# Kernel tuning notes

Hardware: AMD Instinct MI355X
Metric: run time of the kernel (lower is better)

## Reference

```python
import jax, jax.numpy as jnp
import numpy as np

H, KV, D, WIN = 16, 4, 128, 1024


def _rope(x, cos, sin):
    # x: [B, H, S, D]; cos/sin: [1, 1, S, D//2]
    d = x.shape[-1] // 2
    x1, x2 = x[..., :d], x[..., d:]
    S = x.shape[2]
    c, s = cos[:, :, :S], sin[:, :, :S]
    return jnp.concatenate([x1 * c + x2 * s, -x1 * s + x2 * c], axis=-1)


def _rms_norm(x):
    eps = jnp.finfo(x.dtype).eps
    return x * jax.lax.rsqrt(jnp.mean(jnp.square(x), axis=-1, keepdims=True) + eps)


def setup_inputs() -> dict:
    key = jax.random.key(0)
    ks = jax.random.split(key, 7)
    B, S, E = 2, 2048, 2048
    return {
        "x": jax.random.normal(ks[0], (B, S, E), jnp.float32),
        "cos": jax.random.normal(ks[1], (1, 1, S, D // 2), jnp.float32),
        "sin": jax.random.normal(ks[2], (1, 1, S, D // 2), jnp.float32),
        "Wq": jax.random.normal(ks[3], (H * D, E), jnp.float32) * 0.02,
        "Wk": jax.random.normal(ks[4], (KV * D, E), jnp.float32) * 0.02,
        "Wv": jax.random.normal(ks[5], (KV * D, E), jnp.float32) * 0.02,
        "Wo": jax.random.normal(ks[6], (E, H * D), jnp.float32) * 0.02,
    }


def reference(x, cos, sin, Wq, Wk, Wv, Wo):
    B, S, E = x.shape
    rep = H // KV
    # projections -> [B, heads, S, D]
    q = (x @ Wq.T).reshape(B, S, H, D).transpose(0, 2, 1, 3)
    k = (x @ Wk.T).reshape(B, S, KV, D).transpose(0, 2, 1, 3)
    v = (x @ Wv.T).reshape(B, S, KV, D).transpose(0, 2, 1, 3)
    # GQA: materialize repeated K/V heads (matches repeat_interleave)
    k = jnp.repeat(k, rep, axis=1)
    v = jnp.repeat(v, rep, axis=1)
    # RoPE then QK RMSNorm (no learned scale)
    q = _rms_norm(_rope(q, cos, sin))
    k = _rms_norm(_rope(k, cos, sin))
    scores = jnp.einsum("bhqd,bhkd->bhqk", q, k) * (D ** -0.5)
    # causal & sliding-window mask
    i = jnp.arange(S)[:, None]
    j = jnp.arange(S)[None, :]
    mask = (i >= j) & (jnp.abs(i - j) < WIN)
    scores = jnp.where(mask[None, None], scores, -jnp.inf)
    attn = jax.nn.softmax(scores, axis=-1)
    out = jnp.einsum("bhqk,bhkd->bhqd", attn, v)
    out = out.transpose(0, 2, 1, 3).reshape(B, S, H * D)
    return out @ Wo.T
```

## Files before the change

### kernel.cpp

```cpp
#include <hip/hip_runtime.h>
#include <stdint.h>

using bf16 = __bf16;
typedef __bf16 bf16x8 __attribute__((ext_vector_type(8)));
typedef __bf16 bf16x4 __attribute__((ext_vector_type(4)));
typedef float f32x4 __attribute__((ext_vector_type(4)));

#define H_ 16
#define KV_ 4
#define D_ 128
#define WIN_ 1024
#define B_ 2
#define S_ 2048
#define E_ 2048
#define HD_ 2048

__device__ __forceinline__ void gld_lds16(const void* gptr, void* lptr) {
    __builtin_amdgcn_global_load_lds(
        (__attribute__((address_space(1))) void*)(uintptr_t)gptr,
        (__attribute__((address_space(3))) void*)(uintptr_t)lptr, 16, 0, 0);
}

__global__ __launch_bounds__(256) void cvt_all(const float* __restrict__ x,
                                               const float* __restrict__ wq,
                                               const float* __restrict__ wk,
                                               const float* __restrict__ wv,
                                               const float* __restrict__ wo,
                                               bf16* __restrict__ dst) {
    int i = (blockIdx.x * 256 + threadIdx.x) * 4;
    const float* src;
    int off;
    if (i < 8388608)       { src = x;  off = 0; }
    else if (i < 12582912) { src = wq; off = 8388608; }
    else if (i < 13631488) { src = wk; off = 12582912; }
    else if (i < 14680064) { src = wv; off = 13631488; }
    else                   { src = wo; off = 14680064; }
    const float4 v = *(const float4*)(src + (i - off));
    bf16x4 o = {(bf16)v.x, (bf16)v.y, (bf16)v.z, (bf16)v.w};
    *(bf16x4*)(dst + i) = o;
}

#define SCHED0() __builtin_amdgcn_sched_barrier(0)
#define BAR()                          \
    do {                               \
        SCHED0();                      \
        __builtin_amdgcn_s_barrier();  \
        SCHED0();                      \
    } while (0)
#define WAITV(N) asm volatile("s_waitcnt vmcnt(" #N ")" ::: "memory")


template <int NH>
__device__ __forceinline__ void gemm_core32(const bf16* __restrict__ A,
                                            const bf16* __restrict__ W, int m0,
                                            int n0, bf16* sm, f32x4 (&acc)[8][2 * NH]) {
    constexpr int K = 2048;
    const int t = threadIdx.x;
    const int lane = t & 63;
    const int wave = t >> 6;
    const int l15 = lane & 15;
    const int quad = lane >> 4;
    const int wm = (wave & 1) * 128;
    const int wn = (wave >> 1) * (NH * 32);

    bf16* const A0 = sm;
    bf16* const A1 = sm + 8192;
    bf16* const A2 = sm + 16384;
    bf16* const A3 = sm + 24576;
    bf16* const B0 = sm + 32768;
    bf16* const B1 = B0 + NH * 4096;
    bf16* const B2 = B0 + NH * 8192;
    bf16* const B3 = B0 + NH * 12288;

    const bf16* Ap = A + (size_t)(m0 + (t >> 2)) * K + (t & 3) * 8;
    const bf16* Wp = W + (size_t)(n0 + (t >> 2)) * K + (t & 3) * 8;

    auto stA = [&](int u, bf16* d) {
        gld_lds16(Ap + u * 32, d + t * 8);
        gld_lds16(Ap + u * 32 + (size_t)128 * K, d + 4096 + t * 8);
    };
    auto stB = [&](int u, bf16* d) {
        gld_lds16(Wp + u * 32, d + t * 8);
        if constexpr (NH == 2) gld_lds16(Wp + u * 32 + (size_t)128 * K, d + 4096 + t * 8);
    };

    bf16x8 afX[8], afY[8], bfX[2 * NH], bfY[2 * NH];
    auto rdA = [&](const bf16* S, bf16x8 (&af)[8]) {
#pragma unroll
        for (int mi = 0; mi < 8; ++mi)
            af[mi] = *(const bf16x8*)&S[(wm + mi * 16 + l15) * 32 + quad * 8];
    };
    auto rdB = [&](const bf16* S, bf16x8 (&bf)[2 * NH]) {
#pragma unroll
        for (int j = 0; j < 2 * NH; ++j)
            bf[j] = *(const bf16x8*)&S[(wn + j * 16 + l15) * 32 + quad * 8];
    };
    auto MMA = [&](bf16x8 (&af)[8], bf16x8 (&bf)[2 * NH]) {
        __builtin_amdgcn_s_setprio(1);
#pragma unroll
        for (int mi = 0; mi < 8; ++mi)
#pragma unroll
            for (int j = 0; j < 2 * NH; ++j)
                acc[mi][j] = __builtin_amdgcn_mfma_f32_16x16x32_bf16(af[mi], bf[j],
                                                                     acc[mi][j], 0, 0, 0);
        __builtin_amdgcn_s_setprio(0);
    };

#define GT(U, AFM, BFM, AFR, BFR, RA, RB, SA, SB, DOST, WMODE)                      \
    do {                                                                            \
        if (DOST) { stA((U) + 3, SA); stB((U) + 3, SB); }                           \
        MMA(AFM, BFM);                                                              \
        rdA(RA, AFR);                                                               \
        rdB(RB, BFR);                                                               \
        SCHED0();                                                                   \
        if ((WMODE) == 1) {                                                         \
            if constexpr (NH == 2) { WAITV(4); } else { WAITV(3); }                 \
        } else if ((WMODE) == 0) {                                                  \
            WAITV(0);                                                               \
        }                                                                           \
        BAR();                                                                      \
    } while (0)

    stA(0, A0); stB(0, B0);
    stA(1, A1); stB(1, B1);
    stA(2, A2); stB(2, B2);
    SCHED0();
    if constexpr (NH == 2) { WAITV(4); } else { WAITV(3); }
    BAR();
    rdA(A0, afX);
    rdB(B0, bfX);

    for (int it = 0; it < 15; ++it) {
        const int u = it * 4;
        GT(u + 0, afX, bfX, afY, bfY, A1, B1, A3, B3, 1, 1);
        GT(u + 1, afY, bfY, afX, bfX, A2, B2, A0, B0, 1, 1);
        GT(u + 2, afX, bfX, afY, bfY, A3, B3, A1, B1, 1, 1);
        GT(u + 3, afY, bfY, afX, bfX, A0, B0, A2, B2, 1, 1);
    }
    GT(60, afX, bfX, afY, bfY, A1, B1, A3, B3, 1, 1);
    GT(61, afY, bfY, afX, bfX, A2, B2, A0, B0, 0, 0);
    GT(62, afX, bfX, afY, bfY, A3, B3, A1, B1, 0, -1);
    MMA(afY, bfY);
#undef GT
}

__global__ __launch_bounds__(512, 2) void gemm_qkv8(const bf16* __restrict__ A,
                                                    const bf16* __restrict__ W,
                                                    const float* __restrict__ cosp,
                                                    const float* __restrict__ sinp,
                                                    bf16* __restrict__ qn,
                                                    bf16* __restrict__ kn,
                                                    bf16* __restrict__ vt) {
    __shared__ alignas(16) bf16 sm[65536];
    const int flat = blockIdx.y * 16 + blockIdx.x;
    const int swz = (flat & 7) * 24 + (flat >> 3);
    const int m0 = (swz & 15) * 256;
    const int n0 = (swz >> 4) * 256;

    f32x4 acc[8][4] = {};
    gemm_core32<2>(A, W, m0, n0, sm, acc);

    const int t = threadIdx.x;
    const int lane = t & 63;
    const int wave = t >> 6;
    const int l15 = lane & 15;
    const int quad = lane >> 4;
    const int wm = (wave & 1) * 128;
    const int wn = (wave >> 1) * 64;
    bf16* Cs = sm;

#pragma unroll
    for (int ch = 0; ch < 2; ++ch) {
        __syncthreads();
        if (wm == ch * 128) {
#pragma unroll
            for (int mi = 0; mi < 8; ++mi) {
                const int rl = mi * 16 + quad * 4;
#pragma unroll
                for (int nf = 0; nf < 4; ++nf) {
                    const int col = wn + nf * 16 + l15;
#pragma unroll
                    for (int r = 0; r < 4; ++r)
                        Cs[(rl + r) * 264 + col] = (bf16)acc[mi][nf][r];
                }
            }
        }
        __syncthreads();

        if (n0 < 2560) {
            const int rt = t >> 1;
            const int row = rt & 127;
            const int hh = rt >> 7;
            const int half = t & 1;
            const int gr = m0 + ch * 128 + row;
            const int bb = gr >> 11;
            const int s = gr & 2047;
            const int unit = (n0 >> 7) + hh;
            const bf16* crow = &Cs[row * 264 + hh * 128 + half * 32];
            const float* cp = cosp + s * 64 + half * 32;
            const float* sp = sinp + s * 64 + half * 32;
            bf16x8 xa[4], xb2[4];
#pragma unroll
            for (int u = 0; u < 4; ++u) {
                xa[u] = *(const bf16x8*)(crow + u * 8);
                xb2[u] = *(const bf16x8*)(crow + 64 + u * 8);
            }
            float y1[32], y2[32], ss = 0.0f;
#pragma unroll
            for (int u = 0; u < 4; ++u)
#pragma unroll
                for (int e = 0; e < 8; ++e) {
                    const int jj = u * 8 + e;
                    const float x1 = (float)xa[u][e];
                    const float x2 = (float)xb2[u][e];
                    const float c = cp[jj];
                    const float sn = sp[jj];
                    y1[jj] = x1 * c + x2 * sn;
                    y2[jj] = x2 * c - x1 * sn;
                    ss += y1[jj] * y1[jj] + y2[jj] * y2[jj];
                }
            ss += __shfl_xor(ss, 1, 64);
            float rr = rsqrtf(ss * (1.0f / 128.0f) + 1.1920929e-7f);
            bf16* dst;
            if (unit < 16) {
                rr *= 0.12751740f;
                dst = qn + ((size_t)(bb * H_ + unit) * S_ + s) * 128 + half * 32;
            } else {
                dst = kn + ((size_t)(bb * KV_ + (unit - 16)) * S_ + s) * 128 + half * 32;
            }
#pragma unroll
            for (int u = 0; u < 4; ++u) {
                bf16x8 p1, p2;
#pragma unroll
                for (int e = 0; e < 8; ++e) {
                    p1[e] = (bf16)(y1[u * 8 + e] * rr);
                    p2[e] = (bf16)(y2[u * 8 + e] * rr);
                }
                *(bf16x8*)(dst + u * 8) = p1;
                *(bf16x8*)(dst + 64 + u * 8) = p2;
            }
        } else {
            const int hh = t >> 8;
            const int d = (t >> 1) & 127;
            const int sl0 = (t & 1) * 64;
            const int jv = (n0 >> 7) + hh - 20;
            const int base = m0 + ch * 128;
            const int bb = base >> 11;
            const int sW = (base & 2047) + sl0;
            bf16* vdst = vt + ((size_t)(bb * KV_ + jv) * 128 + d) * S_ + sW;
#pragma unroll
            for (int u = 0; u < 8; ++u) {
                bf16x8 pk;
#pragma unroll
                for (int e = 0; e < 8; ++e)
                    pk[e] = Cs[(sl0 + u * 8 + e) * 264 + hh * 128 + d];
                *(bf16x8*)(vdst + u * 8) = pk;
            }
        }
    }
}

__global__ __launch_bounds__(512, 2) void gemm_bt8(const bf16* __restrict__ A,
                                                   const bf16* __restrict__ W,
                                                   float* __restrict__ C, int K,
                                                   int ldc) {
    __shared__ alignas(16) bf16 sm[49152];
    const int flat = blockIdx.y * 16 + blockIdx.x;
    const int swz = (flat & 7) * 32 + (flat >> 3);
    const int m0 = (swz & 15) * 256;
    const int n0 = (swz >> 4) * 128;

    f32x4 acc[8][2] = {};
    gemm_core32<1>(A, W, m0, n0, sm, acc);

    const int t = threadIdx.x;
    const int lane = t & 63;
    const int l15 = lane & 15;
    const int quad = lane >> 4;
    const int wave = t >> 6;
    const int wm = (wave & 1) * 128;
    const int wn = (wave >> 1) * 32;
#pragma unroll
    for (int mi = 0; mi < 8; ++mi) {
        const int row = m0 + wm + mi * 16 + quad * 4;
#pragma unroll
        for (int j = 0; j < 2; ++j) {
            const int col = n0 + wn + j * 16 + l15;
#pragma unroll
            for (int r = 0; r < 4; ++r) C[(size_t)(row + r) * ldc + col] = acc[mi][j][r];
        }
    }
}

__global__ __launch_bounds__(256, 4) void attn_fwd(const bf16* __restrict__ Qn,
                                                   const bf16* __restrict__ Kn,
                                                   const bf16* __restrict__ Vt,
                                                   bf16* __restrict__ Out) {
    __shared__ alignas(16) bf16 Ks[64 * 128];
    __shared__ alignas(16) bf16 Vs[128 * 64];
    __shared__ alignas(16) bf16 Ps[4 * 16 * 64];

    const int t = threadIdx.x;
    const int lane = t & 63;
    const int wave = t >> 6;
    const int l15 = lane & 15;
    const int quad = lane >> 4;
    const int swz = l15 & 7;
    const int qb0 = blockIdx.x * 64;
    const int h = blockIdx.y;
    const int b = blockIdx.z;
    const int hk = h >> 2;
    const int qw0 = qb0 + wave * 16;

    const bf16* qbase = Qn + ((size_t)((b * H_ + h) * S_) + qw0 + l15) * 128;
    bf16x8 qf[4];
#pragma unroll
    for (int c4 = 0; c4 < 4; ++c4) qf[c4] = *(const bf16x8*)(qbase + c4 * 32 + quad * 8);

    f32x4 o[8] = {};
    float m = -1e30f, lsum = 0.0f;

    const bf16* kroot = Kn + (size_t)((b * KV_ + hk) * S_) * 128;
    const bf16* vroot = Vt + (size_t)((b * KV_ + hk) * 128) * S_;

    const int ku = (t & 15) ^ ((t >> 4) & 7);
    const int krow = t >> 4;
    const int vu = (t & 7) ^ ((t >> 3) & 7);
    const int vrow = t >> 3;
    const bf16* kst = kroot + (size_t)krow * 128 + ku * 8;
    const bf16* vst = vroot + (size_t)vrow * S_ + vu * 8;
    bf16* ksl = &Ks[t * 8];
    bf16* vsl = &Vs[t * 8];

    int lo = qb0 - (WIN_ - 1);
    if (lo < 0) lo = 0;
    const int kb_start = lo & ~63;
    const int kb_end = qb0 + 64;

    for (int kb = kb_start; kb < kb_end; kb += 64) {
#pragma unroll
        for (int c = 0; c < 4; ++c) gld_lds16(kst + (size_t)(kb + c * 16) * 128, ksl + c * 2048);
#pragma unroll
        for (int c = 0; c < 4; ++c) gld_lds16(vst + (size_t)(c * 32) * S_ + kb, vsl + c * 2048);
        __syncthreads();

        const bool wave_active = (kb + 63 >= qw0 - (WIN_ - 1));
        if (wave_active) {
            f32x4 sacc[4] = {};
#pragma unroll
            for (int c4 = 0; c4 < 4; ++c4)
#pragma unroll
                for (int kblk = 0; kblk < 4; ++kblk) {
                    bf16x8 kf = *(const bf16x8*)&Ks[(kblk * 16 + l15) * 128 +
                                                    (((c4 * 4 + quad) ^ swz) * 8)];
                    sacc[kblk] =
                        __builtin_amdgcn_mfma_f32_16x16x32_bf16(kf, qf[c4], sacc[kblk], 0, 0, 0);
                }

            const int q = qw0 + l15;
            float sv[16];
            const bool interior = (kb + 63 <= qw0) && (kb >= qw0 + 15 - (WIN_ - 1));
            if (interior) {
#pragma unroll
                for (int kblk = 0; kblk < 4; ++kblk)
#pragma unroll
                    for (int r = 0; r < 4; ++r) sv[kblk * 4 + r] = sacc[kblk][r];
            } else {
#pragma unroll
                for (int kblk = 0; kblk < 4; ++kblk)
#pragma unroll
                    for (int r = 0; r < 4; ++r) {
                        const int key = kb + kblk * 16 + quad * 4 + r;
                        const bool valid = (key <= q) && (q - key < WIN_);
                        sv[kblk * 4 + r] = valid ? sacc[kblk][r] : -1e30f;
                    }
            }
            float mc = sv[0];
#pragma unroll
            for (int i = 1; i < 16; ++i) mc = fmaxf(mc, sv[i]);
            mc = fmaxf(mc, __shfl_xor(mc, 16, 64));
            mc = fmaxf(mc, __shfl_xor(mc, 32, 64));
            const float mnew = fmaxf(m, mc);
            const float al = __builtin_amdgcn_exp2f(m - mnew);
            float ls = 0.0f;
#pragma unroll
            for (int i = 0; i < 16; ++i) {
                sv[i] = __builtin_amdgcn_exp2f(sv[i] - mnew);
                ls += sv[i];
            }
            ls += __shfl_xor(ls, 16, 64);
            ls += __shfl_xor(ls, 32, 64);
            lsum = lsum * al + ls;
            m = mnew;
#pragma unroll
            for (int dblk = 0; dblk < 8; ++dblk) o[dblk] *= al;

            bf16* pw = &Ps[wave * 1024 + l15 * 64];
#pragma unroll
            for (int kblk = 0; kblk < 4; ++kblk) {
                bf16x4 pb = {(bf16)sv[kblk * 4 + 0], (bf16)sv[kblk * 4 + 1],
                             (bf16)sv[kblk * 4 + 2], (bf16)sv[kblk * 4 + 3]};
                const int phys = (kblk * 2 + (quad >> 1)) ^ swz;
                *(bf16x4*)&pw[phys * 8 + (quad & 1) * 4] = pb;
            }
#pragma unroll
            for (int kc = 0; kc < 2; ++kc) {
                const int up = ((kc * 4 + quad) ^ swz) * 8;
                bf16x8 pfv = *(const bf16x8*)&pw[up];
#pragma unroll
                for (int dblk = 0; dblk < 8; ++dblk) {
                    bf16x8 vf = *(const bf16x8*)&Vs[(dblk * 16 + l15) * 64 + up];
                    o[dblk] = __builtin_amdgcn_mfma_f32_16x16x32_bf16(vf, pfv, o[dblk], 0, 0, 0);
                }
            }
        }
        __syncthreads();
    }

    const float inv = 1.0f / lsum;
    const int q = qw0 + l15;
    bf16* ob = Out + (size_t)(b * S_ + q) * HD_ + h * 128;
#pragma unroll
    for (int dblk = 0; dblk < 8; ++dblk) {
        bf16x4 ov = {(bf16)(o[dblk][0] * inv), (bf16)(o[dblk][1] * inv),
                     (bf16)(o[dblk][2] * inv), (bf16)(o[dblk][3] * inv)};
        *(bf16x4*)&ob[dblk * 16 + quad * 4] = ov;
    }
}

extern "C" void kernel_launch(void* const* d_in, const int* in_sizes, int n_in, void* d_out,
                              int out_size, void* d_ws, size_t ws_size, hipStream_t stream) {
    const float* x = (const float*)d_in[0];
    const float* cosp = (const float*)d_in[1];
    const float* sinp = (const float*)d_in[2];
    const float* Wq = (const float*)d_in[3];
    const float* Wk = (const float*)d_in[4];
    const float* Wv = (const float*)d_in[5];
    const float* Wo = (const float*)d_in[6];
    float* out = (float*)d_out;

    constexpr size_t MB = 1ull << 20;
    char* ws = (char*)d_ws;
    bf16* xb    = (bf16*)(ws + 0);
    bf16* wqkv  = (bf16*)(ws + 16 * MB);
    bf16* wo    = (bf16*)(ws + 28 * MB);
    bf16* qn    = (bf16*)(ws + 40 * MB);
    bf16* kn    = (bf16*)(ws + 56 * MB);
    bf16* vt    = (bf16*)(ws + 60 * MB);
    bf16* attnb = (bf16*)(ws + 64 * MB);

    cvt_all<<<18432, 256, 0, stream>>>(x, Wq, Wk, Wv, Wo, xb);
    gemm_qkv8<<<dim3(16, 12), 512, 0, stream>>>(xb, wqkv, cosp, sinp, qn, kn, vt);
    attn_fwd<<<dim3(32, 16, 2), 256, 0, stream>>>(qn, kn, vt, attnb);
    gemm_bt8<<<dim3(16, 16), 512, 0, stream>>>(attnb, wo, out, 2048, 2048);
}
```

Measured before the change: 277.7 us.

## Share K/V tiles across two GQA heads per block, swizzle GEMM LDS

Each attention block now runs 512 threads covering two query heads that share one KV head, so every K/V tile staged in LDS serves twice as many waves and K/V global traffic is halved. The staging is redistributed across eight waves, and MFMA sections get raised wave priority. The GEMM core also XOR-swizzles the LDS column chunk used for the A/B tiles, both when loading and when reading fragments, to reduce bank conflicts. Risks: larger blocks lower scheduling flexibility and occupancy, and the grid has half as many blocks.

```diff
diff --git a/kernel.cpp b/kernel.cpp
--- a/kernel.cpp
+++ b/kernel.cpp
@@ -60,6 +60,7 @@
     const int wave = t >> 6;
     const int l15 = lane & 15;
     const int quad = lane >> 4;
+    const int fs2 = (l15 >> 1) & 3;
     const int wm = (wave & 1) * 128;
     const int wn = (wave >> 1) * (NH * 32);
 
@@ -72,8 +73,8 @@
     bf16* const B2 = B0 + NH * 8192;
     bf16* const B3 = B0 + NH * 12288;
 
-    const bf16* Ap = A + (size_t)(m0 + (t >> 2)) * K + (t & 3) * 8;
-    const bf16* Wp = W + (size_t)(n0 + (t >> 2)) * K + (t & 3) * 8;
+    const bf16* Ap = A + (size_t)(m0 + (t >> 2)) * K + ((t & 3) ^ ((t >> 3) & 3)) * 8;
+    const bf16* Wp = W + (size_t)(n0 + (t >> 2)) * K + ((t & 3) ^ ((t >> 3) & 3)) * 8;
 
     auto stA = [&](int u, bf16* d) {
         gld_lds16(Ap + u * 32, d + t * 8);
@@ -88,12 +89,12 @@
     auto rdA = [&](const bf16* S, bf16x8 (&af)[8]) {
 #pragma unroll
         for (int mi = 0; mi < 8; ++mi)
-            af[mi] = *(const bf16x8*)&S[(wm + mi * 16 + l15) * 32 + quad * 8];
+            af[mi] = *(const bf16x8*)&S[(wm + mi * 16 + l15) * 32 + (quad ^ fs2) * 8];
     };
     auto rdB = [&](const bf16* S, bf16x8 (&bf)[2 * NH]) {
 #pragma unroll
         for (int j = 0; j < 2 * NH; ++j)
-            bf[j] = *(const bf16x8*)&S[(wn + j * 16 + l15) * 32 + quad * 8];
+            bf[j] = *(const bf16x8*)&S[(wn + j * 16 + l15) * 32 + (quad ^ fs2) * 8];
     };
     auto MMA = [&](bf16x8 (&af)[8], bf16x8 (&bf)[2 * NH]) {
         __builtin_amdgcn_s_setprio(1);
@@ -292,13 +293,13 @@
     }
 }
 
-__global__ __launch_bounds__(256, 4) void attn_fwd(const bf16* __restrict__ Qn,
+__global__ __launch_bounds__(512, 4) void attn_fwd(const bf16* __restrict__ Qn,
                                                    const bf16* __restrict__ Kn,
                                                    const bf16* __restrict__ Vt,
                                                    bf16* __restrict__ Out) {
     __shared__ alignas(16) bf16 Ks[64 * 128];
     __shared__ alignas(16) bf16 Vs[128 * 64];
-    __shared__ alignas(16) bf16 Ps[4 * 16 * 64];
+    __shared__ alignas(16) bf16 Ps[8 * 16 * 64];
 
     const int t = threadIdx.x;
     const int lane = t & 63;
@@ -307,10 +308,10 @@
     const int quad = lane >> 4;
     const int swz = l15 & 7;
     const int qb0 = blockIdx.x * 64;
-    const int h = blockIdx.y;
+    const int h = blockIdx.y * 2 + (wave >> 2);
     const int b = blockIdx.z;
-    const int hk = h >> 2;
-    const int qw0 = qb0 + wave * 16;
+    const int hk = blockIdx.y >> 1;
+    const int qw0 = qb0 + (wave & 3) * 16;
 
     const bf16* qbase = Qn + ((size_t)((b * H_ + h) * S_) + qw0 + l15) * 128;
     bf16x8 qf[4];
@@ -323,14 +324,18 @@
     const bf16* kroot = Kn + (size_t)((b * KV_ + hk) * S_) * 128;
     const bf16* vroot = Vt + (size_t)((b * KV_ + hk) * 128) * S_;
 
-    const int ku = (t & 15) ^ ((t >> 4) & 7);
-    const int krow = t >> 4;
-    const int vu = (t & 7) ^ ((t >> 3) & 7);
-    const int vrow = t >> 3;
-    const bf16* kst = kroot + (size_t)krow * 128 + ku * 8;
-    const bf16* vst = vroot + (size_t)vrow * S_ + vu * 8;
-    bf16* ksl = &Ks[t * 8];
-    bf16* vsl = &Vs[t * 8];
+    auto stage = [&](int kb) {
+#pragma unroll
+        for (int c = 0; c < 2; ++c) {
+            const int mchunk = wave * 2 + c;
+            const int kr = 4 * mchunk + (lane >> 4);
+            gld_lds16(kroot + (size_t)(kb + kr) * 128 + ((lane & 15) ^ (kr & 7)) * 8,
+                      &Ks[mchunk * 512 + lane * 8]);
+            const int vr = 8 * mchunk + (lane >> 3);
+            gld_lds16(vroot + (size_t)vr * S_ + kb + ((lane & 7) ^ (vr & 7)) * 8,
+                      &Vs[mchunk * 512 + lane * 8]);
+        }
+    };
 
     int lo = qb0 - (WIN_ - 1);
     if (lo < 0) lo = 0;
@@ -338,15 +343,13 @@
     const int kb_end = qb0 + 64;
 
     for (int kb = kb_start; kb < kb_end; kb += 64) {
-#pragma unroll
-        for (int c = 0; c < 4; ++c) gld_lds16(kst + (size_t)(kb + c * 16) * 128, ksl + c * 2048);
-#pragma unroll
-        for (int c = 0; c < 4; ++c) gld_lds16(vst + (size_t)(c * 32) * S_ + kb, vsl + c * 2048);
+        stage(kb);
         __syncthreads();
 
         const bool wave_active = (kb + 63 >= qw0 - (WIN_ - 1));
         if (wave_active) {
             f32x4 sacc[4] = {};
+            __builtin_amdgcn_s_setprio(1);
 #pragma unroll
             for (int c4 = 0; c4 < 4; ++c4)
 #pragma unroll
@@ -356,6 +359,7 @@
                     sacc[kblk] =
                         __builtin_amdgcn_mfma_f32_16x16x32_bf16(kf, qf[c4], sacc[kblk], 0, 0, 0);
                 }
+            __builtin_amdgcn_s_setprio(0);
 
             const int q = qw0 + l15;
             float sv[16];
@@ -403,6 +407,7 @@
                 const int phys = (kblk * 2 + (quad >> 1)) ^ swz;
                 *(bf16x4*)&pw[phys * 8 + (quad & 1) * 4] = pb;
             }
+            __builtin_amdgcn_s_setprio(1);
 #pragma unroll
             for (int kc = 0; kc < 2; ++kc) {
                 const int up = ((kc * 4 + quad) ^ swz) * 8;
@@ -413,6 +418,7 @@
                     o[dblk] = __builtin_amdgcn_mfma_f32_16x16x32_bf16(vf, pfv, o[dblk], 0, 0, 0);
                 }
             }
+            __builtin_amdgcn_s_setprio(0);
         }
         __syncthreads();
     }
@@ -451,6 +457,6 @@
 
     cvt_all<<<18432, 256, 0, stream>>>(x, Wq, Wk, Wv, Wo, xb);
     gemm_qkv8<<<dim3(16, 12), 512, 0, stream>>>(xb, wqkv, cosp, sinp, qn, kn, vt);
-    attn_fwd<<<dim3(32, 16, 2), 256, 0, stream>>>(qn, kn, vt, attnb);
+    attn_fwd<<<dim3(32, 8, 2), 512, 0, stream>>>(qn, kn, vt, attnb);
     gemm_bt8<<<dim3(16, 16), 512, 0, stream>>>(attnb, wo, out, 2048, 2048);
 }
```

New measurement: 276.5 us. Within noise of the previous version (-0.4%).
